# Optimization experiments

Measured on AMD Instinct MI355X. Metric: run time of the kernel, lower is better.

The kernel has to match this reference:

```python
import jax, jax.numpy as jnp
import numpy as np

B, H, T, DH = 1, 16, 2048, 64
D = 64  # neighbors per query


def setup_inputs() -> dict:
    key = jax.random.key(0)
    k1, k2, k3, k4, k5, k6 = jax.random.split(key, 6)
    q = jax.random.normal(k1, (B, H, T, DH), dtype=jnp.float32)
    k = jax.random.normal(k2, (B, H, T, DH), dtype=jnp.float32)
    v = jax.random.normal(k3, (B, H, T, DH), dtype=jnp.float32)
    edge_type_bias = jax.random.normal(k4, (4,), dtype=jnp.float32) * 0.1
    neigh_idx = jax.random.randint(k5, (B, H, T, D), 0, T, dtype=jnp.int32)
    edge_type = jax.random.randint(k6, (B, H, T, D), 0, 5, dtype=jnp.int32)
    return {"q": q, "k": k, "v": v, "edge_type_bias": edge_type_bias,
            "neigh_idx": neigh_idx, "edge_type": edge_type}


def _gather_neighbors(x, idx):
    # x: [B,H,T,dh], idx: [B,H,T,D] -> [B,H,T,D,dh]
    return jax.vmap(jax.vmap(lambda xs, ii: xs[ii]))(x, idx)


def reference(q, k, v, edge_type_bias, neigh_idx, edge_type):
    b, h, t, dh = q.shape
    # safe_neighbor_idx: clamp out-of-range indices for the gather
    safe_idx = jnp.clip(neigh_idx, 0, t - 1)
    # causal_neighbor_mask: neighbor j valid iff 0 <= j <= i (original order)
    pos = jnp.arange(t, dtype=neigh_idx.dtype)[None, None, :, None]
    mask = (neigh_idx >= 0) & (neigh_idx <= pos)  # [B,H,T,D]
    k_g = _gather_neighbors(k, safe_idx)  # [B,H,T,D,dh]
    v_g = _gather_neighbors(v, safe_idx)  # [B,H,T,D,dh]
    scores = jnp.einsum('bhte,bhtde->bhtd', q, k_g) / jnp.sqrt(jnp.float32(dh))
    # edge-type bias: table [0, bias0..bias3] indexed by edge_type in {0..4}
    full_bias = jnp.concatenate([jnp.zeros((1,), jnp.float32), edge_type_bias])
    scores = scores + full_bias[edge_type]
    # stable masked softmax (fully-masked rows -> all-zero weights)
    neg = jnp.finfo(scores.dtype).min
    s = jnp.where(mask, scores, neg)
    m = jnp.max(s, axis=-1, keepdims=True)
    e = jnp.exp(s - m) * mask.astype(scores.dtype)
    denom = jnp.sum(e, axis=-1, keepdims=True)
    weights = e / jnp.maximum(denom, 1e-20)
    out = jnp.einsum('bhtd,bhtde->bhte', weights, v_g).astype(v.dtype)
    return out
```

## Files before the change

### kernel.cpp

```cpp
#include <hip/hip_runtime.h>
#include <math.h>


#define T_DIM 2048
#define DH    64
#define NB    64
#define WPB   4

__global__ __launch_bounds__(WPB * 64)
void wayfinder_attn_kernel(const float* __restrict__ q,
                           const float* __restrict__ k,
                           const float* __restrict__ v,
                           const float* __restrict__ etb,
                           const int*   __restrict__ neigh_idx,
                           const int*   __restrict__ edge_type,
                           float*       __restrict__ out)
{
    __shared__ int   j_s[WPB][NB];
    __shared__ float w_s[WPB][NB];

    const int lane = threadIdx.x & 63;
    const int wave = threadIdx.x >> 6;
    const int wq   = blockIdx.x * WPB + wave;
    const int t    = wq & (T_DIM - 1);
    const long long qbase    = (long long)wq * DH;
    const long long headbase = (long long)(wq - t) * DH;

    const long long nbase = (long long)wq * NB;
    const int raw = neigh_idx[nbase + lane];
    const int et  = edge_type[nbase + lane];
    const bool valid = (raw >= 0) && (raw <= t);
    const int  sj   = min(max(raw, 0), T_DIM - 1);
    j_s[wave][lane] = sj;

    const int c = lane & 15;
    const int g = lane >> 4;
    const float4 qv = *(const float4*)(q + qbase + c * 4);

    int jarr[16];
    {
        const int4* jg = (const int4*)&j_s[wave][g * 16];
        *(int4*)&jarr[0]  = jg[0];
        *(int4*)&jarr[4]  = jg[1];
        *(int4*)&jarr[8]  = jg[2];
        *(int4*)&jarr[12] = jg[3];
    }

    const float* __restrict__ khead = k + headbase;
    float mydot = 0.f;
    #pragma unroll
    for (int i = 0; i < 16; ++i) {
        const float4 kv = *(const float4*)(khead + (long long)jarr[i] * DH + c * 4);
        float p = kv.x * qv.x + kv.y * qv.y + kv.z * qv.z + kv.w * qv.w;
        p += __shfl_xor(p, 1, 64);
        p += __shfl_xor(p, 2, 64);
        p += __shfl_xor(p, 4, 64);
        p += __shfl_xor(p, 8, 64);
        if (c == i) mydot = p;
    }

    const float bias  = (et != 0) ? etb[et - 1] : 0.f;
    const float score = valid ? (mydot * 0.125f + bias) : -INFINITY;

    float m = score;
    #pragma unroll
    for (int o = 32; o > 0; o >>= 1) m = fmaxf(m, __shfl_xor(m, o, 64));
    const float e = valid ? __expf(score - m) : 0.f;
    float s = e;
    #pragma unroll
    for (int o = 32; o > 0; o >>= 1) s += __shfl_xor(s, o, 64);
    const float w = e / fmaxf(s, 1e-20f);
    w_s[wave][lane] = w;

    const float* __restrict__ vhead = v + headbase;
    float acc = 0.f;
    #pragma unroll
    for (int d4 = 0; d4 < 16; ++d4) {
        const float4 wd = *(const float4*)&w_s[wave][d4 * 4];
        const int4   jd = *(const int4*)&j_s[wave][d4 * 4];
        acc += wd.x * vhead[(long long)jd.x * DH + lane];
        acc += wd.y * vhead[(long long)jd.y * DH + lane];
        acc += wd.z * vhead[(long long)jd.z * DH + lane];
        acc += wd.w * vhead[(long long)jd.w * DH + lane];
    }
    out[qbase + lane] = acc;
}

extern "C" void kernel_launch(void* const* d_in, const int* in_sizes, int n_in,
                              void* d_out, int out_size, void* d_ws, size_t ws_size,
                              hipStream_t stream)
{
    const float* q   = (const float*)d_in[0];
    const float* k   = (const float*)d_in[1];
    const float* v   = (const float*)d_in[2];
    const float* etb = (const float*)d_in[3];
    const int* neigh_idx = (const int*)d_in[4];
    const int* edge_type = (const int*)d_in[5];
    float* out = (float*)d_out;

    const int total_queries = 16 * T_DIM;
    const int blocks = total_queries / WPB;
    hipLaunchKernelGGL(wayfinder_attn_kernel, dim3(blocks), dim3(WPB * 64),
                       0, stream, q, k, v, etb, neigh_idx, edge_type, out);
}
```

Baseline: 136.9 us.

## Pre-convert K/V to bf16 and compact valid neighbors before gather

Adds a pre-pass kernel that truncates K and V to bf16 into the workspace, so the attention kernel gathers half the bytes per neighbor. The attention kernel also compacts causally valid neighbors with a ballot and prefix popcount, skipping K/V loads for masked entries, which is about half of them on random indices. It also changes the lane mapping (8 lanes per key row, 16-lane quarters for the V accumulation). The trade-off is an extra full pass over K and V each call, plus lower precision from truncating rather than rounding, which may exceed tolerance.

```diff
diff --git a/kernel.cpp b/kernel.cpp
--- a/kernel.cpp
+++ b/kernel.cpp
@@ -6,15 +6,138 @@
 #define DH    64
 #define NB    64
 #define WPB   4
+#define KV_ELEMS (16 * T_DIM * DH)
+
+__global__ __launch_bounds__(256)
+void convert_kv_kernel(const float* __restrict__ k, const float* __restrict__ v,
+                       unsigned int* __restrict__ ws)
+{
+    const int tid = blockIdx.x * 256 + threadIdx.x;
+    unsigned int* kh = ws;
+    unsigned int* vh = ws + (KV_ELEMS / 2);
+    const float4 kv = *(const float4*)(k + (long long)tid * 4);
+    const float4 vv = *(const float4*)(v + (long long)tid * 4);
+    uint2 pk, pv;
+    pk.x = (__float_as_uint(kv.x) >> 16) | (__float_as_uint(kv.y) & 0xffff0000u);
+    pk.y = (__float_as_uint(kv.z) >> 16) | (__float_as_uint(kv.w) & 0xffff0000u);
+    pv.x = (__float_as_uint(vv.x) >> 16) | (__float_as_uint(vv.y) & 0xffff0000u);
+    pv.y = (__float_as_uint(vv.z) >> 16) | (__float_as_uint(vv.w) & 0xffff0000u);
+    *(uint2*)(kh + tid * 2) = pk;
+    *(uint2*)(vh + tid * 2) = pv;
+}
+
+__device__ __forceinline__ float bflo(unsigned int u) { return __uint_as_float(u << 16); }
+__device__ __forceinline__ float bfhi(unsigned int u) { return __uint_as_float(u & 0xffff0000u); }
 
 __global__ __launch_bounds__(WPB * 64)
-void wayfinder_attn_kernel(const float* __restrict__ q,
-                           const float* __restrict__ k,
-                           const float* __restrict__ v,
-                           const float* __restrict__ etb,
-                           const int*   __restrict__ neigh_idx,
-                           const int*   __restrict__ edge_type,
-                           float*       __restrict__ out)
+void wayfinder_attn_bf16(const float* __restrict__ q,
+                         const unsigned int* __restrict__ kvws,
+                         const float* __restrict__ etb,
+                         const int*   __restrict__ neigh_idx,
+                         const int*   __restrict__ edge_type,
+                         float*       __restrict__ out)
+{
+    __shared__ int   j_s[WPB][NB];
+    __shared__ float b_s[WPB][NB];
+    __shared__ float w_s[WPB][NB];
+
+    const int lane = threadIdx.x & 63;
+    const int wave = threadIdx.x >> 6;
+    const int wq   = blockIdx.x * WPB + wave;
+    const int t    = wq & (T_DIM - 1);
+    const int qbase    = wq * DH;
+    const int headbase = (wq - t) * DH;
+    const unsigned int* __restrict__ kh = kvws + (headbase >> 1);
+    const unsigned int* __restrict__ vh = kvws + (KV_ELEMS / 2) + (headbase >> 1);
+
+    j_s[wave][lane] = 0;
+    b_s[wave][lane] = 0.f;
+
+    const int raw = neigh_idx[wq * NB + lane];
+    const int et  = edge_type[wq * NB + lane];
+    const bool valid = (raw >= 0) && (raw <= t);
+    const int  sj    = min(max(raw, 0), T_DIM - 1);
+    const float bias = (et != 0) ? etb[et - 1] : 0.f;
+
+    const unsigned long long vb = __ballot(valid);
+    const int nv  = __popcll(vb);
+    const int pos = __popcll(vb & ((1ull << lane) - 1ull));
+    if (valid) { j_s[wave][pos] = sj; b_s[wave][pos] = bias; }
+
+    const int c8 = lane & 7;
+    const int g8 = lane >> 3;
+    const float4 qv0 = *(const float4*)(q + qbase + c8 * 8);
+    const float4 qv1 = *(const float4*)(q + qbase + c8 * 8 + 4);
+
+    int jarr[8];
+    {
+        const int4* jg = (const int4*)&j_s[wave][g8 * 8];
+        *(int4*)&jarr[0] = jg[0];
+        *(int4*)&jarr[4] = jg[1];
+    }
+    const int mycnt = nv - g8 * 8;
+    float mydot = 0.f;
+    #pragma unroll
+    for (int i = 0; i < 8; ++i) {
+        if (i < mycnt) {
+            const uint4 u = *(const uint4*)(kh + jarr[i] * 32 + c8 * 4);
+            float p = bflo(u.x) * qv0.x + bfhi(u.x) * qv0.y
+                    + bflo(u.y) * qv0.z + bfhi(u.y) * qv0.w
+                    + bflo(u.z) * qv1.x + bfhi(u.z) * qv1.y
+                    + bflo(u.w) * qv1.z + bfhi(u.w) * qv1.w;
+            p += __shfl_xor(p, 1, 64);
+            p += __shfl_xor(p, 2, 64);
+            p += __shfl_xor(p, 4, 64);
+            if (c8 == i) mydot = p;
+        }
+    }
+
+    const bool dval = lane < nv;
+    const float score = dval ? (mydot * 0.125f + b_s[wave][lane]) : -INFINITY;
+    float m = score;
+    #pragma unroll
+    for (int o = 32; o > 0; o >>= 1) m = fmaxf(m, __shfl_xor(m, o, 64));
+    const float e = dval ? __expf(score - m) : 0.f;
+    float s = e;
+    #pragma unroll
+    for (int o = 32; o > 0; o >>= 1) s += __shfl_xor(s, o, 64);
+    const float w = e / fmaxf(s, 1e-20f);
+    w_s[wave][lane] = w;
+
+    const int qw   = lane >> 4;
+    const int lp16 = lane & 15;
+    float a0 = 0.f, a1 = 0.f, a2 = 0.f, a3 = 0.f;
+    for (int base = 0; base < nv; base += 16) {
+        #pragma unroll
+        for (int ii = 0; ii < 4; ++ii) {
+            const int e2 = base + ii * 4 + qw;
+            const float we = w_s[wave][e2];
+            const int   je = j_s[wave][e2];
+            const uint2 uv = *(const uint2*)(vh + je * 32 + lp16 * 2);
+            a0 += we * bflo(uv.x);
+            a1 += we * bfhi(uv.x);
+            a2 += we * bflo(uv.y);
+            a3 += we * bfhi(uv.y);
+        }
+    }
+    a0 += __shfl_xor(a0, 16, 64);  a1 += __shfl_xor(a1, 16, 64);
+    a2 += __shfl_xor(a2, 16, 64);  a3 += __shfl_xor(a3, 16, 64);
+    a0 += __shfl_xor(a0, 32, 64);  a1 += __shfl_xor(a1, 32, 64);
+    a2 += __shfl_xor(a2, 32, 64);  a3 += __shfl_xor(a3, 32, 64);
+    if (lane < 16) {
+        float4 o; o.x = a0; o.y = a1; o.z = a2; o.w = a3;
+        *(float4*)(out + qbase + lane * 4) = o;
+    }
+}
+
+__global__ __launch_bounds__(WPB * 64)
+void wayfinder_attn_f32(const float* __restrict__ q,
+                        const float* __restrict__ k,
+                        const float* __restrict__ v,
+                        const float* __restrict__ etb,
+                        const int*   __restrict__ neigh_idx,
+                        const int*   __restrict__ edge_type,
+                        float*       __restrict__ out)
 {
     __shared__ int   j_s[WPB][NB];
     __shared__ float w_s[WPB][NB];
@@ -100,6 +223,16 @@
 
     const int total_queries = 16 * T_DIM;
     const int blocks = total_queries / WPB;
-    hipLaunchKernelGGL(wayfinder_attn_kernel, dim3(blocks), dim3(WPB * 64),
-                       0, stream, q, k, v, etb, neigh_idx, edge_type, out);
-}
+    const size_t need = (size_t)KV_ELEMS * 2 * sizeof(unsigned short);
+
+    if (ws_size >= need) {
+        unsigned int* ws = (unsigned int*)d_ws;
+        hipLaunchKernelGGL(convert_kv_kernel, dim3(KV_ELEMS / 4 / 256), dim3(256),
+                           0, stream, k, v, ws);
+        hipLaunchKernelGGL(wayfinder_attn_bf16, dim3(blocks), dim3(WPB * 64),
+                           0, stream, q, ws, etb, neigh_idx, edge_type, out);
+    } else {
+        hipLaunchKernelGGL(wayfinder_attn_f32, dim3(blocks), dim3(WPB * 64),
+                           0, stream, q, k, v, etb, neigh_idx, edge_type, out);
+    }
+}
```

After: 123.7 us. -9.7%, faster.
